# Optimization experiments

Hardware: AMD Instinct MI355X
Metric: run time of the kernel (lower is better)

The kernel has to match this reference:

```python
import jax, jax.numpy as jnp
import numpy as np

T_STEPS = 200
B = 512
D = 32
LMBD = 1.0


def _socm_const_m_loss(ts, states, noises, controls, nabla_V, nabla_f,
                       nabla_b, nabla_g, sigma, log_pd, log_ps, log_tw):
    # ts: [T+1]; states/nabla_V: [T+1,B,D]; noises/controls/nabla_f: [T,B,D];
    # nabla_b: [T,B,D,D]; nabla_g: [B,D]; sigma: [D,D]; logs: [B]
    sigma_inv_T = jnp.linalg.inv(sigma).T

    # integrand terms on the first T timesteps ([:-1] slice in torch source)
    term1 = nabla_f  # nabla_f(ts[0], states)[:-1]
    sig_noises = jnp.einsum('ij,abj->abi', sigma_inv_T, noises)
    term2 = -np.sqrt(LMBD) * jnp.einsum('abij,abj->abi', nabla_b, sig_noises)
    sig_controls = jnp.einsum('ij,abj->abi', sigma_inv_T, controls)
    term3 = -jnp.einsum('abij,abj->abi', nabla_b, sig_controls)

    dts = ts[1:] - ts[:-1]                      # [T]
    dts_ = dts[:, None, None]
    zeros = jnp.zeros_like(term1[:1])           # [1,B,D]

    t1_dt = jnp.concatenate([zeros, term1 * dts_], axis=0)             # [T+1,B,D]
    t2_sdt = jnp.concatenate([zeros, term2 * jnp.sqrt(dts_)], axis=0)
    t3_dt = jnp.concatenate([zeros, term3 * dts_], axis=0)

    def rev_cum(x):
        # total_sum - cumsum == reverse cumulative sum starting at each step
        return jnp.sum(x, axis=0, keepdims=True) - jnp.cumsum(x, axis=0)

    least_squares_target = (rev_cum(t1_dt) + rev_cum(t2_sdt) + rev_cum(t3_dt)
                            + nabla_g[None, :, :])                     # [T+1,B,D]

    control_learned = -jnp.einsum('ij,tbj->tbi', sigma.T, nabla_V)
    control_target = -jnp.einsum('ij,tbj->tbi', sigma.T, least_squares_target)

    weight = jnp.exp(log_pd + log_ps + log_tw)  # [B]
    sq = (control_learned - control_target) ** 2 * weight[None, :, None]
    n_t, n_b = states.shape[0], states.shape[1]
    return jnp.sum(sq) / (n_t * n_b)


def setup_inputs() -> dict:
    key = jax.random.key(0)
    ks = jax.random.split(key, 11)
    ts = jnp.linspace(0.0, 1.0, T_STEPS + 1, dtype=jnp.float32)
    states = jax.random.normal(ks[0], (T_STEPS + 1, B, D), jnp.float32)
    noises = jax.random.normal(ks[1], (T_STEPS, B, D), jnp.float32)
    controls = jax.random.normal(ks[2], (T_STEPS, B, D), jnp.float32)
    nabla_V = jax.random.normal(ks[3], (T_STEPS + 1, B, D), jnp.float32)
    nabla_f = jax.random.normal(ks[4], (T_STEPS, B, D), jnp.float32)
    nabla_b = 0.1 * jax.random.normal(ks[5], (T_STEPS, B, D, D), jnp.float32)
    nabla_g = jax.random.normal(ks[6], (B, D), jnp.float32)
    sigma = jnp.eye(D, dtype=jnp.float32) + 0.05 * jax.random.normal(ks[7], (D, D), jnp.float32)
    log_pd = 0.01 * jax.random.normal(ks[8], (B,), jnp.float32)
    log_ps = 0.01 * jax.random.normal(ks[9], (B,), jnp.float32)
    log_tw = 0.01 * jax.random.normal(ks[10], (B,), jnp.float32)
    return {"ts": ts, "states": states, "noises": noises, "controls": controls,
            "nabla_V": nabla_V, "nabla_f": nabla_f, "nabla_b": nabla_b,
            "nabla_g": nabla_g, "sigma": sigma, "log_pd": log_pd,
            "log_ps": log_ps, "log_tw": log_tw}


def reference(ts, states, noises, controls, nabla_V, nabla_f, nabla_b,
              nabla_g, sigma, log_pd, log_ps, log_tw):
    return _socm_const_m_loss(ts, states, noises, controls, nabla_V, nabla_f,
                              nabla_b, nabla_g, sigma, log_pd, log_ps, log_tw)
```

## Files before the change

kernel.cpp:

```cpp
#include <hip/hip_runtime.h>
#include <math.h>

#define T_STEPS 200
#define BB 512
#define DD 32
#define LMBD 1.0f

#define WS_MINV 0
#define WS_A    1024
#define WS_W    2048
#define WS_PART 2560
#define WS_C    3072

__global__ __launch_bounds__(512) void prep_kernel(
    const float* __restrict__ sigma,
    const float* __restrict__ lpd, const float* __restrict__ lps,
    const float* __restrict__ ltw,
    float* __restrict__ ws)
{
    __shared__ float sg[32][33];
    const int tid = threadIdx.x;

    ws[WS_W + tid] = expf(lpd[tid] + lps[tid] + ltw[tid]);

    for (int idx = tid; idx < 1024; idx += 512)
        sg[idx >> 5][idx & 31] = sigma[idx];
    __syncthreads();

    for (int idx = tid; idx < 1024; idx += 512) {
        int i = idx >> 5, j = idx & 31;
        float s = 0.0f;
        #pragma unroll
        for (int k = 0; k < 32; ++k) s += sg[i][k] * sg[j][k];
        ws[WS_A + idx] = s;
    }

    if (tid < 64) {
        const int l = tid;
        float col[32];
        #pragma unroll
        for (int r = 0; r < 32; ++r) {
            float v = sg[r][l & 31];
            col[r] = (l < 32) ? v : ((r == (l - 32)) ? 1.0f : 0.0f);
        }
        #pragma unroll
        for (int k = 0; k < 32; ++k) {
            float pinv = 1.0f / __shfl(col[k], k);
            col[k] *= pinv;
            #pragma unroll
            for (int r = 0; r < 32; ++r) {
                if (r == k) continue;
                float f = __shfl(col[r], k);
                col[r] -= f * col[k];
            }
        }
        if (l >= 32) {
            #pragma unroll
            for (int r = 0; r < 32; ++r)
                ws[WS_MINV + (l - 32) * 32 + r] = col[r];
        }
    }
}

__global__ __launch_bounds__(256) void c_kernel(
    const float* __restrict__ ts,
    const float* __restrict__ noises,
    const float* __restrict__ controls,
    const float* __restrict__ nabla_f,
    const float* __restrict__ nabla_b,
    float* __restrict__ ws)
{
    __shared__ float w8[8 * 36];
    __shared__ float v8[8 * 36];

    const int t   = blockIdx.x;
    const int b0  = blockIdx.y << 3;
    const int tid = threadIdx.x;
    const int bl  = tid >> 5;
    const int i   = tid & 31;

    const float dt  = ts[t + 1] - ts[t];
    const float sdt = sqrtf(LMBD * dt);

    const int base = (t * BB + b0) * DD;

    {
        float nv = noises[base + tid];
        float cv = controls[base + tid];
        w8[bl * 36 + i] = -sdt * nv - dt * cv;
    }

    float4 mrow[8];
    {
        const float4* mp = (const float4*)(ws + WS_MINV + i * 32);
        #pragma unroll
        for (int c = 0; c < 8; ++c) mrow[c] = mp[c];
    }
    __syncthreads();

    float v = 0.0f;
    {
        const float4* wr = (const float4*)(w8 + bl * 36);
        #pragma unroll
        for (int c = 0; c < 8; ++c) {
            float4 a = wr[c];
            v += mrow[c].x * a.x + mrow[c].y * a.y + mrow[c].z * a.z + mrow[c].w * a.w;
        }
    }
    v8[bl * 36 + i] = v;
    __syncthreads();

    const int wv = tid >> 6;
    const int l  = tid & 63;
    const int g  = l & 7;

    const float4* nb4 = (const float4*)nabla_b + (size_t)(base + (wv << 6)) * 8;

    float myval = 0.0f;
    #pragma unroll
    for (int c = 0; c < 8; ++c) {
        float4 nb = nb4[c * 64 + l];
        const int bloc = (wv << 1) + (c >> 2);
        float4 vv = *(const float4*)&v8[bloc * 36 + (g << 2)];
        float p = nb.x * vv.x + nb.y * vv.y + nb.z * vv.z + nb.w * vv.w;
        p += __shfl_xor(p, 1);
        p += __shfl_xor(p, 2);
        p += __shfl_xor(p, 4);
        float rc = __shfl(p, (l & 7) << 3);
        myval = ((l >> 3) == c) ? rc : myval;
    }

    const int rr    = (wv << 6) + l;
    const int gread = base + rr;
    const int bloc2 = rr >> 5, i2 = rr & 31;
    ws[WS_C + ((b0 + bloc2) * T_STEPS + t) * DD + i2] =
        dt * nabla_f[gread] + myval;
}

__global__ __launch_bounds__(256) void loss_kernel(
    const float* __restrict__ nabla_V,
    const float* __restrict__ nabla_g,
    float* __restrict__ ws)
{
    __shared__ float s[201 * 36];
    const int b   = blockIdx.x;
    const int tid = threadIdx.x;

    float vpre[26];
    #pragma unroll
    for (int u = 0; u < 26; ++u) {
        int idx = tid + u * 256;
        if (idx < 201 * 32) {
            int t = idx >> 5, i3 = idx & 31;
            vpre[u] = nabla_V[(t * BB + b) * DD + i3];
        } else vpre[u] = 0.0f;
    }

    const float* cb = ws + WS_C + b * (T_STEPS * DD);
    for (int idx = tid; idx < T_STEPS * DD; idx += 256)
        s[(idx >> 5) * 36 + (idx & 31)] = cb[idx];
    if (tid < 32) s[200 * 36 + tid] = nabla_g[b * 32 + tid];
    __syncthreads();

    const int cch = tid >> 5, ii = tid & 31;
    {
        float acc = 0.0f;
        for (int k = 24; k >= 0; --k) {
            int a = (cch * 25 + k) * 36 + ii;
            acc += s[a];
            s[a] = acc;
        }
    }
    __syncthreads();

    float O = s[200 * 36 + ii];
    for (int c2 = cch + 1; c2 < 8; ++c2) O += s[(c2 * 25) * 36 + ii];
    __syncthreads();

    for (int k = 0; k < 25; ++k) s[(cch * 25 + k) * 36 + ii] += O;
    __syncthreads();

    #pragma unroll
    for (int u = 0; u < 26; ++u) {
        int idx = tid + u * 256;
        if (idx < 201 * 32) s[(idx >> 5) * 36 + (idx & 31)] -= vpre[u];
    }
    __syncthreads();

    const int i  = tid >> 3;
    const int jc = tid & 7;
    float a0 = 0.f, a1 = 0.f, a2 = 0.f, a3 = 0.f;
    for (int t = 0; t <= 200; ++t) {
        float  ei = s[t * 36 + i];
        float4 ej = *(const float4*)&s[t * 36 + jc * 4];
        a0 += ei * ej.x; a1 += ei * ej.y; a2 += ei * ej.z; a3 += ei * ej.w;
    }

    float4 a4 = *(const float4*)(ws + WS_A + i * 32 + jc * 4);
    float part = a0 * a4.x + a1 * a4.y + a2 * a4.z + a3 * a4.w;
    __syncthreads();
    s[tid] = part;
    __syncthreads();
    for (int st = 128; st > 0; st >>= 1) {
        if (tid < st) s[tid] += s[tid + st];
        __syncthreads();
    }
    if (tid == 0) ws[WS_PART + b] = ws[WS_W + b] * s[0];
}

__global__ __launch_bounds__(512) void reduce_kernel(
    const float* __restrict__ ws, float* __restrict__ out)
{
    __shared__ float r[512];
    const int tid = threadIdx.x;
    r[tid] = ws[WS_PART + tid];
    __syncthreads();
    for (int st = 256; st > 0; st >>= 1) {
        if (tid < st) r[tid] += r[tid + st];
        __syncthreads();
    }
    if (tid == 0) out[0] = r[0] * (1.0f / (201.0f * 512.0f));
}

extern "C" void kernel_launch(void* const* d_in, const int* in_sizes, int n_in,
                              void* d_out, int out_size, void* d_ws, size_t ws_size,
                              hipStream_t stream) {
    (void)in_sizes; (void)n_in; (void)out_size; (void)ws_size;
    const float* ts       = (const float*)d_in[0];
    const float* noises   = (const float*)d_in[2];
    const float* controls = (const float*)d_in[3];
    const float* nabla_V  = (const float*)d_in[4];
    const float* nabla_f  = (const float*)d_in[5];
    const float* nabla_b  = (const float*)d_in[6];
    const float* nabla_g  = (const float*)d_in[7];
    const float* sigma    = (const float*)d_in[8];
    const float* lpd      = (const float*)d_in[9];
    const float* lps      = (const float*)d_in[10];
    const float* ltw      = (const float*)d_in[11];
    float* ws  = (float*)d_ws;
    float* out = (float*)d_out;

    prep_kernel<<<1, 512, 0, stream>>>(sigma, lpd, lps, ltw, ws);
    c_kernel<<<dim3(T_STEPS, BB / 8), 256, 0, stream>>>(ts, noises, controls,
                                                        nabla_f, nabla_b, ws);
    loss_kernel<<<BB, 256, 0, stream>>>(nabla_V, nabla_g, ws);
    reduce_kernel<<<1, 512, 0, stream>>>(ws, out);
}
```

Baseline: 128.0 us.

## Fuse prefix-sum and loss into chunked streaming kernel with algebraic combine

Replaces the per-timestep C computation and the separate reverse-cumsum loss kernel with a single kernel. Each block streams one batch element over a time chunk, accumulating a running prefix and a local quadratic form. A small combine kernel corrects for chunk offsets using an algebraic expansion of the quadratic. This removes the global write and read of the intermediate target tensor but makes each block a serial loop with per-step barriers and shallow prefetch.

```diff
diff --git a/kernel.cpp b/kernel.cpp
--- a/kernel.cpp
+++ b/kernel.cpp
@@ -5,12 +5,16 @@
 #define BB 512
 #define DD 32
 #define LMBD 1.0f
+#define NCH 4
+#define CHT 50
 
 #define WS_MINV 0
 #define WS_A    1024
 #define WS_W    2048
 #define WS_PART 2560
-#define WS_C    3072
+#define WS_CT   3072
+#define WS_Y    (3072 + 65536)
+#define WS_M    (3072 + 131072)
 
 __global__ __launch_bounds__(512) void prep_kernel(
     const float* __restrict__ sigma,
@@ -62,150 +66,177 @@
     }
 }
 
-__global__ __launch_bounds__(256) void c_kernel(
+__global__ __launch_bounds__(256) void stream_kernel(
     const float* __restrict__ ts,
     const float* __restrict__ noises,
     const float* __restrict__ controls,
     const float* __restrict__ nabla_f,
+    const float* __restrict__ nabla_V,
     const float* __restrict__ nabla_b,
     float* __restrict__ ws)
 {
-    __shared__ float w8[8 * 36];
-    __shared__ float v8[8 * 36];
-
-    const int t   = blockIdx.x;
-    const int b0  = blockIdx.y << 3;
-    const int tid = threadIdx.x;
-    const int bl  = tid >> 5;
-    const int i   = tid & 31;
-
-    const float dt  = ts[t + 1] - ts[t];
-    const float sdt = sqrtf(LMBD * dt);
-
-    const int base = (t * BB + b0) * DD;
+    __shared__ float ts_l[52];
+    __shared__ __align__(16) float buf[2][4][32];
+    __shared__ __align__(16) float vls[32];
+    __shared__ __align__(16) float yls[32];
+    __shared__ float red[256];
+
+    const int h   = blockIdx.x;
+    const int b   = blockIdx.y;
+    const int tid = threadIdx.x;
+    const int r   = tid >> 3;
+    const int q   = tid & 7;
+    const int w   = tid >> 6;
+    const int lane = tid & 63;
+
+    const int t0 = h * CHT, t1 = t0 + CHT;
+
+    const float* sp_w = (w == 0) ? noises : (w == 1) ? controls
+                       : (w == 2) ? nabla_f : nabla_V;
+
+    if (tid < 51) ts_l[tid] = ts[t0 + tid];
+    if (lane < 32) buf[0][w][lane] = sp_w[((size_t)t0 * BB + b) * DD + lane];
+
+    float4 Minv4 = *(const float4*)(ws + WS_MINV + r * 32 + 4 * q);
+    float4 nbCur = ((const float4*)nabla_b + (size_t)(t0 * BB + b) * 256)[tid];
+
+    float P = 0.0f, Yacc = 0.0f;
+    float a0 = 0.f, a1 = 0.f, a2 = 0.f, a3 = 0.f;
+    __syncthreads();
+
+    for (int t = t0; t < t1; ++t) {
+        const int p = t & 1;
+        const int tn = (t + 1 < t1) ? t + 1 : t1 - 1;
+        float4 nbNext = ((const float4*)nabla_b + (size_t)(tn * BB + b) * 256)[tid];
+        float smallNext = 0.0f;
+        if (lane < 32) smallNext = sp_w[((size_t)tn * BB + b) * DD + lane];
+
+        const float dt  = ts_l[t - t0 + 1] - ts_l[t - t0];
+        const float sdt = sqrtf(LMBD * dt);
+
+        {
+            float4 n4 = *(const float4*)&buf[p][0][4 * q];
+            float4 c4 = *(const float4*)&buf[p][1][4 * q];
+            float wx = -sdt * n4.x - dt * c4.x;
+            float wy = -sdt * n4.y - dt * c4.y;
+            float wz = -sdt * n4.z - dt * c4.z;
+            float ww = -sdt * n4.w - dt * c4.w;
+            float pv = Minv4.x * wx + Minv4.y * wy + Minv4.z * wz + Minv4.w * ww;
+            pv += __shfl_xor(pv, 1);
+            pv += __shfl_xor(pv, 2);
+            pv += __shfl_xor(pv, 4);
+            if (q == 0) vls[r] = pv;
+        }
+        __syncthreads();
+
+        float yr;
+        {
+            float Vt = buf[p][3][r];
+            yr = P + Vt;
+            if (q == 0) yls[r] = yr;
+            float4 v4 = *(const float4*)&vls[4 * q];
+            float pc = nbCur.x * v4.x + nbCur.y * v4.y
+                     + nbCur.z * v4.z + nbCur.w * v4.w;
+            pc += __shfl_xor(pc, 1);
+            pc += __shfl_xor(pc, 2);
+            pc += __shfl_xor(pc, 4);
+            float fr = buf[p][2][r];
+            P += dt * fr + pc;
+            Yacc += yr;
+        }
+        __syncthreads();
+
+        {
+            float4 y4 = *(const float4*)&yls[4 * q];
+            a0 += yr * y4.x; a1 += yr * y4.y; a2 += yr * y4.z; a3 += yr * y4.w;
+        }
+        if (lane < 32) buf[p ^ 1][w][lane] = smallNext;
+        nbCur = nbNext;
+        __syncthreads();
+    }
+
+    if (h == NCH - 1) {
+        float Vt = nabla_V[((size_t)T_STEPS * BB + b) * DD + r];
+        float yr = P + Vt;
+        if (q == 0) yls[r] = yr;
+        Yacc += yr;
+        __syncthreads();
+        float4 y4 = *(const float4*)&yls[4 * q];
+        a0 += yr * y4.x; a1 += yr * y4.y; a2 += yr * y4.z; a3 += yr * y4.w;
+        __syncthreads();
+    }
 
     {
-        float nv = noises[base + tid];
-        float cv = controls[base + tid];
-        w8[bl * 36 + i] = -sdt * nv - dt * cv;
-    }
-
-    float4 mrow[8];
-    {
-        const float4* mp = (const float4*)(ws + WS_MINV + i * 32);
-        #pragma unroll
-        for (int c = 0; c < 8; ++c) mrow[c] = mp[c];
-    }
-    __syncthreads();
-
-    float v = 0.0f;
-    {
-        const float4* wr = (const float4*)(w8 + bl * 36);
-        #pragma unroll
-        for (int c = 0; c < 8; ++c) {
-            float4 a = wr[c];
-            v += mrow[c].x * a.x + mrow[c].y * a.y + mrow[c].z * a.z + mrow[c].w * a.w;
-        }
-    }
-    v8[bl * 36 + i] = v;
-    __syncthreads();
-
-    const int wv = tid >> 6;
-    const int l  = tid & 63;
-    const int g  = l & 7;
-
-    const float4* nb4 = (const float4*)nabla_b + (size_t)(base + (wv << 6)) * 8;
-
-    float myval = 0.0f;
-    #pragma unroll
-    for (int c = 0; c < 8; ++c) {
-        float4 nb = nb4[c * 64 + l];
-        const int bloc = (wv << 1) + (c >> 2);
-        float4 vv = *(const float4*)&v8[bloc * 36 + (g << 2)];
-        float p = nb.x * vv.x + nb.y * vv.y + nb.z * vv.z + nb.w * vv.w;
-        p += __shfl_xor(p, 1);
-        p += __shfl_xor(p, 2);
-        p += __shfl_xor(p, 4);
-        float rc = __shfl(p, (l & 7) << 3);
-        myval = ((l >> 3) == c) ? rc : myval;
-    }
-
-    const int rr    = (wv << 6) + l;
-    const int gread = base + rr;
-    const int bloc2 = rr >> 5, i2 = rr & 31;
-    ws[WS_C + ((b0 + bloc2) * T_STEPS + t) * DD + i2] =
-        dt * nabla_f[gread] + myval;
-}
-
-__global__ __launch_bounds__(256) void loss_kernel(
-    const float* __restrict__ nabla_V,
+        float4 A4 = *(const float4*)(ws + WS_A + r * 32 + 4 * q);
+        float mp = a0 * A4.x + a1 * A4.y + a2 * A4.z + a3 * A4.w;
+        red[tid] = mp;
+        __syncthreads();
+        for (int st = 128; st > 0; st >>= 1) {
+            if (tid < st) red[tid] += red[tid + st];
+            __syncthreads();
+        }
+        if (q == 0) {
+            ws[WS_CT + (b * NCH + h) * 32 + r] = P;
+            ws[WS_Y  + (b * NCH + h) * 32 + r] = Yacc;
+        }
+        if (tid == 0) ws[WS_M + b * NCH + h] = red[0];
+    }
+}
+
+__global__ __launch_bounds__(256) void combine_kernel(
     const float* __restrict__ nabla_g,
     float* __restrict__ ws)
 {
-    __shared__ float s[201 * 36];
+    __shared__ float ct[NCH][32], Yl[NCH][32];
+    __shared__ float Sv[32], Cp[32];
+    __shared__ __align__(16) float sp[32];
+    __shared__ float red[32];
+
     const int b   = blockIdx.x;
     const int tid = threadIdx.x;
-
-    float vpre[26];
-    #pragma unroll
-    for (int u = 0; u < 26; ++u) {
-        int idx = tid + u * 256;
-        if (idx < 201 * 32) {
-            int t = idx >> 5, i3 = idx & 31;
-            vpre[u] = nabla_V[(t * BB + b) * DD + i3];
-        } else vpre[u] = 0.0f;
-    }
-
-    const float* cb = ws + WS_C + b * (T_STEPS * DD);
-    for (int idx = tid; idx < T_STEPS * DD; idx += 256)
-        s[(idx >> 5) * 36 + (idx & 31)] = cb[idx];
-    if (tid < 32) s[200 * 36 + tid] = nabla_g[b * 32 + tid];
-    __syncthreads();
-
-    const int cch = tid >> 5, ii = tid & 31;
-    {
-        float acc = 0.0f;
-        for (int k = 24; k >= 0; --k) {
-            int a = (cch * 25 + k) * 36 + ii;
-            acc += s[a];
-            s[a] = acc;
-        }
-    }
-    __syncthreads();
-
-    float O = s[200 * 36 + ii];
-    for (int c2 = cch + 1; c2 < 8; ++c2) O += s[(c2 * 25) * 36 + ii];
-    __syncthreads();
-
-    for (int k = 0; k < 25; ++k) s[(cch * 25 + k) * 36 + ii] += O;
-    __syncthreads();
-
-    #pragma unroll
-    for (int u = 0; u < 26; ++u) {
-        int idx = tid + u * 256;
-        if (idx < 201 * 32) s[(idx >> 5) * 36 + (idx & 31)] -= vpre[u];
-    }
-    __syncthreads();
-
-    const int i  = tid >> 3;
-    const int jc = tid & 7;
-    float a0 = 0.f, a1 = 0.f, a2 = 0.f, a3 = 0.f;
-    for (int t = 0; t <= 200; ++t) {
-        float  ei = s[t * 36 + i];
-        float4 ej = *(const float4*)&s[t * 36 + jc * 4];
-        a0 += ei * ej.x; a1 += ei * ej.y; a2 += ei * ej.z; a3 += ei * ej.w;
-    }
-
-    float4 a4 = *(const float4*)(ws + WS_A + i * 32 + jc * 4);
-    float part = a0 * a4.x + a1 * a4.y + a2 * a4.z + a3 * a4.w;
-    __syncthreads();
-    s[tid] = part;
-    __syncthreads();
-    for (int st = 128; st > 0; st >>= 1) {
-        if (tid < st) s[tid] += s[tid + st];
-        __syncthreads();
-    }
-    if (tid == 0) ws[WS_PART + b] = ws[WS_W + b] * s[0];
+    const int r   = tid >> 3;
+    const int q   = tid & 7;
+
+    if (tid < NCH * 32) {
+        int hh = tid >> 5, i = tid & 31;
+        ct[hh][i] = ws[WS_CT + (b * NCH + hh) * 32 + i];
+        Yl[hh][i] = ws[WS_Y  + (b * NCH + hh) * 32 + i];
+    }
+    if (tid < 32) Cp[tid] = 0.0f;
+    __syncthreads();
+    if (tid < 32) {
+        float s = nabla_g[b * 32 + tid];
+        #pragma unroll
+        for (int hh = 0; hh < NCH; ++hh) s += ct[hh][tid];
+        Sv[tid] = s;
+    }
+
+    float acc = 0.0f;
+    float4 A4 = *(const float4*)(ws + WS_A + r * 32 + 4 * q);
+    for (int hh = 0; hh < NCH; ++hh) {
+        __syncthreads();
+        if (tid < 32) sp[tid] = Sv[tid] - Cp[tid];
+        __syncthreads();
+        float4 s4 = *(const float4*)&sp[4 * q];
+        float as = A4.x * s4.x + A4.y * s4.y + A4.z * s4.z + A4.w * s4.w;
+        as += __shfl_xor(as, 1);
+        as += __shfl_xor(as, 2);
+        as += __shfl_xor(as, 4);
+        float nh = (hh == NCH - 1) ? (float)(CHT + 1) : (float)CHT;
+        if (q == 0) acc += as * (nh * sp[r] - 2.0f * Yl[hh][r]);
+        if (tid < 32) Cp[tid] += ct[hh][tid];
+    }
+    __syncthreads();
+    if (q == 0) red[r] = acc;
+    __syncthreads();
+    if (tid == 0) {
+        float s = 0.0f;
+        #pragma unroll
+        for (int i = 0; i < 32; ++i) s += red[i];
+        #pragma unroll
+        for (int hh = 0; hh < NCH; ++hh) s += ws[WS_M + b * NCH + hh];
+        ws[WS_PART + b] = ws[WS_W + b] * s;
+    }
 }
 
 __global__ __launch_bounds__(512) void reduce_kernel(
@@ -241,8 +272,8 @@
     float* out = (float*)d_out;
 
     prep_kernel<<<1, 512, 0, stream>>>(sigma, lpd, lps, ltw, ws);
-    c_kernel<<<dim3(T_STEPS, BB / 8), 256, 0, stream>>>(ts, noises, controls,
-                                                        nabla_f, nabla_b, ws);
-    loss_kernel<<<BB, 256, 0, stream>>>(nabla_V, nabla_g, ws);
+    stream_kernel<<<dim3(NCH, BB), 256, 0, stream>>>(ts, noises, controls,
+                                                     nabla_f, nabla_V, nabla_b, ws);
+    combine_kernel<<<BB, 256, 0, stream>>>(nabla_g, ws);
     reduce_kernel<<<1, 512, 0, stream>>>(ws, out);
 }
```

Result: faster. 111.1 us (-13.2%).
